# Optimization experiments

Hardware: AMD Instinct MI355X
Metric: run time of the kernel (lower is better)

## Reference

```python
import jax, jax.numpy as jnp
import numpy as np

NE = 14          # NUM_ELEMENTS
NC = 20          # NUM_CHANNEL
DEN = NE         # density channel
GRV = NE + 1     # gravity channel

# (id, density, gravity) per element, in id order
_ELEMS = [(0,1,1),(1,4,0),(2,3,1),(3,2,1),(4,0,1),(5,4,0),(6,4,0),(7,0,1),(8,4,0),(9,3,1),(10,3,1),(11,2,1),(12,3,1),(13,4,0)]

def _elem_table():
    t = np.zeros((NE, NC), dtype=np.float32)
    for eid, dens, grav in _ELEMS:
        t[eid, eid] = 1.0
        t[eid, DEN] = dens
        t[eid, GRV] = grav
    return jnp.asarray(t)

# torch.roll semantics: get_above(x)[h] = x[h-1] (wrap)
above = lambda x: jnp.roll(x, 1, axis=2)
below = lambda x: jnp.roll(x, -1, axis=2)
left  = lambda x: jnp.roll(x, 1, axis=3)
right = lambda x: jnp.roll(x, -1, axis=3)

def interp2(sa, sb, if_false, if_a, if_b):
    # faithful to torch: (~a & ~b)*f + a*xa + b*xb (bools broadcast-multiply floats)
    return (jnp.logical_and(~sa, ~sb)) * if_false + sa * if_a + sb * if_b

def setup_inputs() -> dict:
    key = jax.random.key(0)
    k1, k2 = jax.random.split(key)
    B, H, W = 8, 512, 512
    ids = jax.random.randint(k1, (B, H, W), 0, NE)
    world = _elem_table()[ids]                 # [B,H,W,NC]
    world = jnp.transpose(world, (0, 3, 1, 2)) # [B,NC,H,W]
    rand_movement = jax.random.uniform(k2, (B, 1, H, W), dtype=jnp.float32)
    return {"world": world, "rand_movement": rand_movement}

def reference(world, rand_movement):
    B, C, H, W = world.shape
    # --- stone support check (conv2d with zero padding, taps at top-left/top-right) ---
    stone = world[:, 9:10]
    p = jnp.pad(stone, ((0, 0), (0, 0), (1, 1), (1, 1)))
    supports = p[:, :, 0:H, 0:W] + p[:, :, 0:H, 2:W + 2]  # stone[h-1,w-1]+stone[h-1,w+1]
    new_grav = (1.0 - stone) * world[:, GRV:GRV + 1] + stone * (supports < 2)
    world = world.at[:, GRV:GRV + 1].set(new_grav)

    # --- vertical gravity passes over densities 0..3 ---
    did_gravity = jnp.zeros((B, 1, H, W), dtype=world.dtype)
    for curr_density in (0, 1, 2, 3):
        density = world[:, DEN:DEN + 1]
        is_density_above_greater = (above(density) - density) > 0
        is_density_below_less = below(is_density_above_greater)
        is_density_current = density == curr_density
        is_density_above_current = above(is_density_current)
        is_gravity = world[:, GRV:GRV + 1] == 1
        is_cb_gravity = jnp.logical_and(below(is_gravity), is_gravity)
        is_ca_gravity = jnp.logical_and(above(is_gravity), is_gravity)
        does_become_below = is_density_current & is_density_below_less & is_cb_gravity
        does_become_above = is_density_above_greater & is_density_above_current & is_ca_gravity
        did_gravity = did_gravity + does_become_above
        world = interp2(does_become_below, does_become_above, world, below(world), above(world))

    # --- diagonal fall for sand (2) and dust (12) ---
    for elem in (2, 12):
        fall_dir = rand_movement > 0.5
        not_did_gravity = did_gravity <= 0
        for fall_left in (True, False):
            g_dir = left if fall_left else right
            g_not = right if fall_left else left
            is_element = world[:, elem:elem + 1] == 1
            is_ar_element = g_not(above(is_element))
            density = world[:, DEN:DEN + 1]
            is_matching_fall = fall_dir if fall_left else ~fall_dir
            is_ar_matching_fall = g_not(above(is_matching_fall))
            is_bl_density_lower = (density - g_dir(below(density))) > 0
            is_ar_density_higher = (g_not(above(density)) - density) > 0
            is_gravity = world[:, GRV:GRV + 1] == 1
            is_bl_gravity = jnp.logical_and(g_dir(below(is_gravity)), is_gravity)
            is_ar_gravity = jnp.logical_and(g_not(above(is_gravity)), is_gravity)
            ndg_bl = jnp.logical_and(g_dir(below(not_did_gravity)), not_did_gravity)
            ndg_ar = jnp.logical_and(g_not(above(not_did_gravity)), not_did_gravity)
            does_become_bl = is_element & ndg_bl & is_matching_fall & is_bl_density_lower & is_bl_gravity
            does_become_ar = is_ar_element & ndg_ar & is_ar_matching_fall & is_ar_density_higher & is_ar_gravity
            world = interp2(does_become_bl, does_become_ar, world, g_dir(below(world)), g_not(above(world)))
    return world
```

## Files before the change

kernel.cpp:

```cpp
#include <hip/hip_runtime.h>
#include <stdint.h>

#define HH 512
#define WW 512
#define PLANE (HH*WW)
#define NCH 20

#define DENS_PACK 0x43233404402341ULL
#define GRAV_PACK 0x1E9Du

__device__ __forceinline__ int dens_of(int e) {
    return (int)((DENS_PACK >> (e * 4)) & 0xFULL);
}

__device__ __forceinline__ uint32_t eqz4(uint32_t x) {
    uint32_t nz = (x | (x >> 1) | (x >> 2) | (x >> 3)) & 0x01010101u;
    return nz ^ 0x01010101u;
}
__device__ __forceinline__ uint32_t gtb(uint32_t a, uint32_t b) {
    uint32_t t = (a | 0x08080808u) - b;
    return ((t + 0x07070707u) & 0x10101010u) >> 4;
}
__device__ __forceinline__ uint32_t bmask(uint32_t b) {
    uint32_t h = b << 7;
    return (h - (h >> 7)) | h;
}

__global__ __launch_bounds__(256) void extract_k(const float* __restrict__ world,
                                                 uint32_t* __restrict__ st) {
    int idx = blockIdx.x * 256 + threadIdx.x;
    int b  = idx >> 16;
    int p4 = idx & 0xFFFF;
    const float4* base = (const float4*)(world + (size_t)b * NCH * PLANE) + p4;
    int e0 = 0, e1 = 0, e2 = 0, e3 = 0;
#pragma unroll
    for (int c = 1; c < 14; ++c) {
        float4 v = base[c * (PLANE / 4)];
        if (v.x != 0.0f) e0 = c;
        if (v.y != 0.0f) e1 = c;
        if (v.z != 0.0f) e2 = c;
        if (v.w != 0.0f) e3 = c;
    }
#define PACK(e) ((uint32_t)((e) | (((GRAV_PACK >> (e)) & 1u) << 4) | (dens_of(e) << 5)))
    st[idx] = PACK(e0) | (PACK(e1) << 8) | (PACK(e2) << 16) | (PACK(e3) << 24);
#undef PACK
}

#define TILE 64
#define HALO_H 9
#define HALO_W 8
#define RH (TILE + 2*HALO_H)
#define RWW 20
#define RWS 21
#define NW (RH*RWW)

__global__ __launch_bounds__(512) void sim_k(const uint8_t* __restrict__ st_in,
                                             const float* __restrict__ rnd,
                                             float* __restrict__ out) {
    __shared__ uint32_t bufA[RH * RWS];
    __shared__ uint32_t bufB[RH * RWS];
    __shared__ uint32_t aux [RH * RWS];

    const int tid = threadIdx.x;
    const int b   = blockIdx.z;
    const int h0  = blockIdx.y * TILE;
    const int w0  = blockIdx.x * TILE;
    const uint8_t* stb = st_in + (size_t)b * PLANE;
    const float*   rb  = rnd   + (size_t)b * PLANE;

    for (int r = tid; r < NW; r += 512) {
        int i = r / RWW, jw = r - i * RWW;
        int gh  = (h0 + i - HALO_H) & (HH - 1);
        int gwb = (w0 + jw * 4 - HALO_W) & (WW - 1);
        bufA[i * RWS + jw] = *(const uint32_t*)(stb + gh * WW + gwb);
        const float* rp = rb + gh * WW + gwb;
        uint32_t aw = 0;
        aw |= (rp[0] > 0.5f) ? 0x00000001u : 0u;
        aw |= (rp[1] > 0.5f) ? 0x00000100u : 0u;
        aw |= (rp[2] > 0.5f) ? 0x00010000u : 0u;
        aw |= (rp[3] > 0.5f) ? 0x01000000u : 0u;
        aux[i * RWS + jw] = aw;
    }
    __syncthreads();

    for (int r = tid; r < NW; r += 512) {
        int i = r / RWW, jw = r - i * RWW;
        uint32_t s = bufA[i * RWS + jw];
        uint32_t stm = eqz4((s & 0x0F0F0F0Fu) ^ 0x09090909u);
        int im = (i > 0) ? i - 1 : 0;
        int jl = (jw > 0) ? jw - 1 : 0;
        int jr = (jw < RWW - 1) ? jw + 1 : RWW - 1;
        uint32_t wU  = bufA[im * RWS + jw];
        uint32_t wUL = bufA[im * RWS + jl];
        uint32_t wUR = bufA[im * RWS + jr];
        uint32_t upL = (wU << 8) | (wUL >> 24);
        uint32_t upR = (wU >> 8) | (wUR << 24);
        uint32_t stL = eqz4((upL & 0x0F0F0F0Fu) ^ 0x09090909u);
        uint32_t stR = eqz4((upR & 0x0F0F0F0Fu) ^ 0x09090909u);
        int gh  = (h0 + i - HALO_H) & (HH - 1);
        int gwb = (w0 + jw * 4 - HALO_W) & (WW - 1);
        uint32_t rowOK = (gh != 0) ? 0x01010101u : 0u;
        uint32_t okL = 0x01010101u ^ ((gwb == 0)      ? 0x00000001u : 0u);
        uint32_t okR = 0x01010101u ^ ((gwb == WW - 4) ? 0x01000000u : 0u);
        uint32_t supL = stL & okL & rowOK;
        uint32_t supR = stR & okR & rowOK;
        uint32_t g2 = 0x01010101u ^ (supL & supR);
        uint32_t ns = (s & ~0x10101010u) | (g2 << 4);
        bufB[i * RWS + jw] = s ^ ((s ^ ns) & bmask(stm));
    }
    __syncthreads();

    uint32_t* cur = bufB;
    uint32_t* nxt = bufA;

    for (int curr = 0; curr < 4; ++curr) {
        const uint32_t crep = (uint32_t)curr * 0x01010101u;
        for (int r = tid; r < NW; r += 512) {
            int i = r / RWW, jw = r - i * RWW;
            int ia = (i > 0) ? i - 1 : 0;
            int ib = (i < RH - 1) ? i + 1 : RH - 1;
            uint32_t s  = cur[i  * RWS + jw];
            uint32_t sa = cur[ia * RWS + jw];
            uint32_t sb = cur[ib * RWS + jw];
            uint32_t d  = (s  >> 5) & 0x07070707u;
            uint32_t da = (sa >> 5) & 0x07070707u;
            uint32_t db = (sb >> 5) & 0x07070707u;
            uint32_t g  = (s  >> 4) & 0x01010101u;
            uint32_t ga = (sa >> 4) & 0x01010101u;
            uint32_t gb = (sb >> 4) & 0x01010101u;
            uint32_t bel = eqz4(d ^ crep)  & gtb(d, db)  & gb & g;
            uint32_t abv = eqz4(da ^ crep) & gtb(da, d)  & ga & g;
            nxt[i * RWS + jw] = s ^ ((s ^ sb) & bmask(bel)) ^ ((s ^ sa) & bmask(abv));
            aux[i * RWS + jw] |= (abv << 1);
        }
        __syncthreads();
        uint32_t* t = cur; cur = nxt; nxt = t;
    }

    for (int pass = 0; pass < 4; ++pass) {
        const int  elem = (pass < 2) ? 2 : 12;
        const bool fl   = ((pass & 1) == 0);
        const uint32_t erep = (uint32_t)elem * 0x01010101u;
        for (int r = tid; r < NW; r += 512) {
            int i = r / RWW, jw = r - i * RWW;
            int ia = (i > 0) ? i - 1 : 0;
            int ib = (i < RH - 1) ? i + 1 : RH - 1;
            int jl = (jw > 0) ? jw - 1 : 0;
            int jr = (jw < RWW - 1) ? jw + 1 : RWW - 1;
            uint32_t s   = cur[i * RWS + jw];
            uint32_t wB  = cur[ib * RWS + jw];
            uint32_t wA  = cur[ia * RWS + jw];
            uint32_t aB  = aux[ib * RWS + jw];
            uint32_t aA  = aux[ia * RWS + jw];
            uint32_t sbl, sar, abl, aar;
            if (fl) {
                uint32_t wBL = cur[ib * RWS + jl], wAR = cur[ia * RWS + jr];
                uint32_t aBL = aux[ib * RWS + jl], aAR = aux[ia * RWS + jr];
                sbl = (wB << 8) | (wBL >> 24);
                sar = (wA >> 8) | (wAR << 24);
                abl = (aB << 8) | (aBL >> 24);
                aar = (aA >> 8) | (aAR << 24);
            } else {
                uint32_t wBR = cur[ib * RWS + jr], wAL = cur[ia * RWS + jl];
                uint32_t aBR = aux[ib * RWS + jr], aAL = aux[ia * RWS + jl];
                sbl = (wB >> 8) | (wBR << 24);
                sar = (wA << 8) | (wAL >> 24);
                abl = (aB >> 8) | (aBR << 24);
                aar = (aA << 8) | (aAL >> 24);
            }
            uint32_t ax = aux[i * RWS + jw];
            uint32_t d   = (s   >> 5) & 0x07070707u;
            uint32_t dbl = (sbl >> 5) & 0x07070707u;
            uint32_t dar = (sar >> 5) & 0x07070707u;
            uint32_t g   = (s   >> 4) & 0x01010101u;
            uint32_t gbl = (sbl >> 4) & 0x01010101u;
            uint32_t gar = (sar >> 4) & 0x01010101u;
            uint32_t ndg   = ((~ax)  >> 1) & 0x01010101u;
            uint32_t ndgbl = ((~abl) >> 1) & 0x01010101u;
            uint32_t ndgar = ((~aar) >> 1) & 0x01010101u;
            uint32_t mtc = (fl ? ax  : ~ax)  & 0x01010101u;
            uint32_t mta = (fl ? aar : ~aar) & 0x01010101u;
            uint32_t eqe  = eqz4((s   & 0x0F0F0F0Fu) ^ erep);
            uint32_t eqer = eqz4((sar & 0x0F0F0F0Fu) ^ erep);
            uint32_t bbl = eqe  & ndgbl & ndg & mtc & gtb(d, dbl)  & gbl & g;
            uint32_t bar = eqer & ndgar & ndg & mta & gtb(dar, d)  & gar & g;
            nxt[i * RWS + jw] = s ^ ((s ^ sbl) & bmask(bbl)) ^ ((s ^ sar) & bmask(bar));
        }
        __syncthreads();
        uint32_t* t = cur; cur = nxt; nxt = t;
    }

    float* ob = out + (size_t)b * NCH * PLANE;
    for (int idx = tid; idx < NCH * 64 * 16; idx += 512) {
        int col4 = idx & 15;
        int row  = (idx >> 4) & 63;
        int c    = idx >> 10;
        uint32_t w = cur[(HALO_H + row) * RWS + (HALO_W / 4) + col4];
        float4 v;
        float* vv = &v.x;
#pragma unroll
        for (int q = 0; q < 4; ++q) {
            uint32_t byte = (w >> (8 * q)) & 0xFFu;
            float val;
            if (c < 14)       val = ((byte & 15u) == (uint32_t)c) ? 1.0f : 0.0f;
            else if (c == 14) val = (float)((byte >> 5) & 7u);
            else if (c == 15) val = (float)((byte >> 4) & 1u);
            else              val = 0.0f;
            vv[q] = val;
        }
        *(float4*)(ob + (size_t)c * PLANE + (size_t)(h0 + row) * WW + (w0 + col4 * 4)) = v;
    }
}

extern "C" void kernel_launch(void* const* d_in, const int* in_sizes, int n_in,
                              void* d_out, int out_size, void* d_ws, size_t ws_size,
                              hipStream_t stream) {
    const float* world = (const float*)d_in[0];
    const float* rnd   = (const float*)d_in[1];
    float* out = (float*)d_out;
    uint32_t* st = (uint32_t*)d_ws;

    extract_k<<<2048, 256, 0, stream>>>(world, st);

    dim3 grid(WW / TILE, HH / TILE, 8);
    sim_k<<<grid, 512, 0, stream>>>((const uint8_t*)st, rnd, out);
}
```

Baseline: 64.13 us.

## Split output expansion into separate kernel and vectorize random loads

The simulation kernel now writes a packed byte-per-cell state to a workspace buffer instead of expanding all 20 float channels itself. A new fully parallel expand kernel reads that packed state and writes the 20-channel float output with one thread per four cells, so the large output write is spread across many more threads and is no longer tied to the 512-block sim grid. The random-movement loads in the halo fill also become single float4 loads. The cost is an extra kernel launch and a round trip through global memory for the packed state.

```diff
diff --git a/kernel.cpp b/kernel.cpp
--- a/kernel.cpp
+++ b/kernel.cpp
@@ -56,7 +56,7 @@
 
 __global__ __launch_bounds__(512) void sim_k(const uint8_t* __restrict__ st_in,
                                              const float* __restrict__ rnd,
-                                             float* __restrict__ out) {
+                                             uint32_t* __restrict__ st_out) {
     __shared__ uint32_t bufA[RH * RWS];
     __shared__ uint32_t bufB[RH * RWS];
     __shared__ uint32_t aux [RH * RWS];
@@ -73,12 +73,12 @@
         int gh  = (h0 + i - HALO_H) & (HH - 1);
         int gwb = (w0 + jw * 4 - HALO_W) & (WW - 1);
         bufA[i * RWS + jw] = *(const uint32_t*)(stb + gh * WW + gwb);
-        const float* rp = rb + gh * WW + gwb;
+        float4 rv = *(const float4*)(rb + gh * WW + gwb);
         uint32_t aw = 0;
-        aw |= (rp[0] > 0.5f) ? 0x00000001u : 0u;
-        aw |= (rp[1] > 0.5f) ? 0x00000100u : 0u;
-        aw |= (rp[2] > 0.5f) ? 0x00010000u : 0u;
-        aw |= (rp[3] > 0.5f) ? 0x01000000u : 0u;
+        aw |= (rv.x > 0.5f) ? 0x00000001u : 0u;
+        aw |= (rv.y > 0.5f) ? 0x00000100u : 0u;
+        aw |= (rv.z > 0.5f) ? 0x00010000u : 0u;
+        aw |= (rv.w > 0.5f) ? 0x01000000u : 0u;
         aux[i * RWS + jw] = aw;
     }
     __syncthreads();
@@ -190,26 +190,51 @@
         uint32_t* t = cur; cur = nxt; nxt = t;
     }
 
-    float* ob = out + (size_t)b * NCH * PLANE;
-    for (int idx = tid; idx < NCH * 64 * 16; idx += 512) {
-        int col4 = idx & 15;
-        int row  = (idx >> 4) & 63;
-        int c    = idx >> 10;
-        uint32_t w = cur[(HALO_H + row) * RWS + (HALO_W / 4) + col4];
+    uint32_t* ob = st_out + (size_t)b * (PLANE / 4);
+    for (int idx = tid; idx < 64 * 16; idx += 512) {
+        int row = idx >> 4, cw = idx & 15;
+        ob[(size_t)(h0 + row) * (WW / 4) + (w0 / 4) + cw] =
+            cur[(HALO_H + row) * RWS + (HALO_W / 4) + cw];
+    }
+}
+
+__global__ __launch_bounds__(256) void expand_k(const uint32_t* __restrict__ st,
+                                                float* __restrict__ out) {
+    int idx = blockIdx.x * 256 + threadIdx.x;
+    uint32_t w = st[idx];
+    int b  = idx >> 16;
+    int p4 = idx & 0xFFFF;
+    float* ob = out + (size_t)b * NCH * PLANE + (size_t)p4 * 4;
+    int e0 = w & 15, e1 = (w >> 8) & 15, e2 = (w >> 16) & 15, e3 = (w >> 24) & 15;
+#pragma unroll
+    for (int c = 0; c < 14; ++c) {
         float4 v;
-        float* vv = &v.x;
+        v.x = (e0 == c) ? 1.0f : 0.0f;
+        v.y = (e1 == c) ? 1.0f : 0.0f;
+        v.z = (e2 == c) ? 1.0f : 0.0f;
+        v.w = (e3 == c) ? 1.0f : 0.0f;
+        *(float4*)(ob + (size_t)c * PLANE) = v;
+    }
+    {
+        float4 v;
+        v.x = (float)((w >> 5)  & 7u);
+        v.y = (float)((w >> 13) & 7u);
+        v.z = (float)((w >> 21) & 7u);
+        v.w = (float)((w >> 29) & 7u);
+        *(float4*)(ob + (size_t)14 * PLANE) = v;
+    }
+    {
+        float4 v;
+        v.x = (float)((w >> 4)  & 1u);
+        v.y = (float)((w >> 12) & 1u);
+        v.z = (float)((w >> 20) & 1u);
+        v.w = (float)((w >> 28) & 1u);
+        *(float4*)(ob + (size_t)15 * PLANE) = v;
+    }
+    float4 z = {0.0f, 0.0f, 0.0f, 0.0f};
 #pragma unroll
-        for (int q = 0; q < 4; ++q) {
-            uint32_t byte = (w >> (8 * q)) & 0xFFu;
-            float val;
-            if (c < 14)       val = ((byte & 15u) == (uint32_t)c) ? 1.0f : 0.0f;
-            else if (c == 14) val = (float)((byte >> 5) & 7u);
-            else if (c == 15) val = (float)((byte >> 4) & 1u);
-            else              val = 0.0f;
-            vv[q] = val;
-        }
-        *(float4*)(ob + (size_t)c * PLANE + (size_t)(h0 + row) * WW + (w0 + col4 * 4)) = v;
-    }
+    for (int c = 16; c < 20; ++c)
+        *(float4*)(ob + (size_t)c * PLANE) = z;
 }
 
 extern "C" void kernel_launch(void* const* d_in, const int* in_sizes, int n_in,
@@ -218,10 +243,13 @@
     const float* world = (const float*)d_in[0];
     const float* rnd   = (const float*)d_in[1];
     float* out = (float*)d_out;
-    uint32_t* st = (uint32_t*)d_ws;
+    uint32_t* st  = (uint32_t*)d_ws;
+    uint32_t* st2 = (uint32_t*)((char*)d_ws + 2*1024*1024);
 
     extract_k<<<2048, 256, 0, stream>>>(world, st);
 
     dim3 grid(WW / TILE, HH / TILE, 8);
-    sim_k<<<grid, 512, 0, stream>>>((const uint8_t*)st, rnd, out);
-}
+    sim_k<<<grid, 512, 0, stream>>>((const uint8_t*)st, rnd, st2);
+
+    expand_k<<<2048, 256, 0, stream>>>(st2, out);
+}
```

Result: slower. 70.39 us (+9.8%).
